# Kernel optimization log

Measured on AMD Instinct MI355X. Metric: run time of the kernel, lower is better.

## Reference

```python
import jax, jax.numpy as jnp
import numpy as np

EPS = 1e-5  # torch BatchNorm1d default eps


def setup_inputs() -> dict:
    key = jax.random.key(0)
    ks = jax.random.split(key, 8)
    F, P = 32, 64            # frames, peds per frame
    B = F * P                # batch = 2048
    E, H, M, D = 64, 128, 512, 1024  # embed, h_dim, pool_mlp_dim, bottleneck
    starts = np.arange(F, dtype=np.int64) * P
    seq_start_end = jnp.asarray(np.stack([starts, starts + P], axis=1))
    inp = {
        "curr_h_states": jax.random.normal(ks[0], (1, B, H), dtype=jnp.float32),
        "curr_pos": jax.random.normal(ks[1], (B, 2), dtype=jnp.float32),
        "seq_start_end": seq_start_end,
        # embedding: Linear(2, E)
        "We": jax.random.normal(ks[2], (2, E), dtype=jnp.float32) * 0.5,
        "be": jnp.zeros((E,), dtype=jnp.float32),
        # mlp layer 1: Linear(E+H, M) + BN(M)
        "W1": jax.random.normal(ks[3], (E + H, M), dtype=jnp.float32) * 0.05,
        "b1": jnp.zeros((M,), dtype=jnp.float32),
        "g1": jnp.ones((M,), dtype=jnp.float32),
        "beta1": jnp.zeros((M,), dtype=jnp.float32),
        # mlp layer 2: Linear(M, D) + BN(D)
        "W2": jax.random.normal(ks[4], (M, D), dtype=jnp.float32) * 0.04,
        "b2": jnp.zeros((D,), dtype=jnp.float32),
        "g2": jnp.ones((D,), dtype=jnp.float32),
        "beta2": jnp.zeros((D,), dtype=jnp.float32),
        # BN running stats (eval mode)
        "rm1": jnp.zeros((M,), dtype=jnp.float32),
        "rv1": jnp.ones((M,), dtype=jnp.float32),
        "rm2": jnp.zeros((D,), dtype=jnp.float32),
        "rv2": jnp.ones((D,), dtype=jnp.float32),
    }
    return inp


def _bn(x, g, beta, rm, rv):
    return g * (x - rm) * jax.lax.rsqrt(rv + EPS) + beta


def reference(curr_h_states, curr_pos, seq_start_end, We, be, W1, b1, g1, beta1,
              W2, b2, g2, beta2, rm1, rv1, rm2, rv2):
    # Equal-size frames: vectorize the per-frame Python loop via a reshape.
    F = seq_start_end.shape[0]
    B = curr_h_states.shape[1]
    P = B // F
    h = curr_h_states[0].reshape(F, P, -1)      # (F, P, H)
    pos = curr_pos.reshape(F, P, 2)             # (F, P, 2)
    # rel_pos[f, i, j] = pos[f, j] - pos[f, i]  (repeat minus repeat_interleave)
    rel = pos[:, None, :, :] - pos[:, :, None, :]          # (F, P, P, 2)
    emb = rel @ We + be                                     # (F, P, P, E)
    h_rep = jnp.broadcast_to(h[:, None, :, :], (F, P, P, h.shape[-1]))
    x = jnp.concatenate([emb, h_rep], axis=-1)              # (F, P, P, E+H)
    x = jax.nn.relu(_bn(x @ W1 + b1, g1, beta1, rm1, rv1))  # (F, P, P, M)
    x = jax.nn.relu(_bn(x @ W2 + b2, g2, beta2, rm2, rv2))  # (F, P, P, D)
    pool_h = x.max(axis=2)                                  # max over j -> (F, P, D)
    return pool_h.reshape(B, -1)                            # (B, D)
```

## Files before the change

kernel.cpp:

```cpp
#include <hip/hip_runtime.h>
#include <hip/hip_bf16.h>
#include <stdint.h>

#define EPS_BN 1e-5f

constexpr int Fn = 32;
constexpr int Pn = 64;
constexpr int Bn = 2048;
constexpr int Hn = 128;
constexpr int En = 64;
constexpr int Mn = 512;
constexpr int Dn = 1024;

using bf16x8  = __attribute__((ext_vector_type(8))) short;
using f32x16  = __attribute__((ext_vector_type(16))) float;

static __device__ __forceinline__ float    bcf(uint32_t u) { return __builtin_bit_cast(float, u); }
static __device__ __forceinline__ uint32_t bcu(float f)    { return __builtin_bit_cast(uint32_t, f); }
static __device__ __forceinline__ unsigned short bfbits(float f) {
  return __builtin_bit_cast(unsigned short, __float2bfloat16(f));
}

static __device__ __forceinline__ void dma16(const uint4* g, const uint4* l) {
  __builtin_amdgcn_global_load_lds(
      (const __attribute__((address_space(1))) unsigned int*)g,
      (__attribute__((address_space(3))) unsigned int*)l, 16, 0, 0);
}

static __device__ __forceinline__ bf16x8 mk_af(uint4 a, uint4 q) {
  uint4 x;
#pragma unroll
  for (int v = 0; v < 4; ++v) {
    uint32_t aw = ((const uint32_t*)&a)[v], qw = ((const uint32_t*)&q)[v];
    float lo = fmaxf(bcf(aw << 16) - bcf(qw << 16), 0.f);
    float hi = fmaxf(bcf(aw) - bcf(qw), 0.f);
    ((uint32_t*)&x)[v] = __builtin_amdgcn_perm(bcu(hi), bcu(lo), 0x07060302u);
  }
  return __builtin_bit_cast(bf16x8, x);
}

__global__ void prep_all(const float* __restrict__ hs, const float* __restrict__ pos,
                         const float* __restrict__ We, const float* __restrict__ be,
                         const float* __restrict__ W1, const float* __restrict__ b1,
                         const float* __restrict__ g1, const float* __restrict__ beta1,
                         const float* __restrict__ rm1, const float* __restrict__ rv1,
                         const float* __restrict__ W2, const float* __restrict__ b2,
                         const float* __restrict__ g2, const float* __restrict__ beta2,
                         const float* __restrict__ rm2, const float* __restrict__ rv2,
                         __hip_bfloat16* __restrict__ Agb, __hip_bfloat16* __restrict__ Qgb,
                         uint4* __restrict__ W2g, float* __restrict__ c2) {
  __shared__ float smem[64 * 65];
  int bid = blockIdx.x, t = threadIdx.x;
  if (bid < 512) {
    int rb = bid * 4, m = t;
    float* hsh = smem;
    float* psh = smem + 512;
    if (t < 4 * Hn) hsh[t] = hs[rb * Hn + t];
    if (t < 8) psh[t] = pos[rb * 2 + t];
    __syncthreads();
    float w0 = 0.f, w1 = 0.f, c = 0.f;
    for (int e = 0; e < En; ++e) {
      float w = W1[e * Mn + m];
      w0 += We[e] * w; w1 += We[En + e] * w; c += be[e] * w;
    }
    c += b1[m];
    float s  = g1[m] * rsqrtf(rv1[m] + EPS_BN);
    float tt = beta1[m] - rm1[m] * s;
    float acc[4];
#pragma unroll
    for (int ri = 0; ri < 4; ++ri) acc[ri] = c;
    for (int e = 0; e < Hn; ++e) {
      float w = W1[(En + e) * Mn + m];
#pragma unroll
      for (int ri = 0; ri < 4; ++ri) acc[ri] += hsh[ri * Hn + e] * w;
    }
#pragma unroll
    for (int ri = 0; ri < 4; ++ri) {
      float q = psh[ri * 2] * w0 + psh[ri * 2 + 1] * w1;
      Agb[(rb + ri) * Mn + m] = __float2bfloat16((acc[ri] + q) * s + tt);
      Qgb[(rb + ri) * Mn + m] = __float2bfloat16(q * s);
    }
  } else {
    int b2i = bid - 512;
    int d0 = (b2i & 15) * 64, k0 = (b2i >> 4) * 64;
    int col = t & 63, row8 = t >> 6;
#pragma unroll
    for (int rr = 0; rr < 8; ++rr) {
      int row = rr * 8 + row8;
      smem[row * 65 + col] = W2[(k0 + row) * Dn + d0 + col];
    }
    __syncthreads();
    int lane = t & 63, q8 = t >> 6;
    int sel_n = q8 & 1, sel_ks = q8 >> 1;
    int dl = sel_n * 32 + (lane & 31), d = d0 + dl;
    float sf = g2[d] * rsqrtf(rv2[d] + EPS_BN);
    int kb = sel_ks * 16 + (lane >> 5) * 8;
    uint32_t wd[4];
#pragma unroll
    for (int h = 0; h < 4; ++h) {
      uint32_t u0 = bfbits(smem[(kb + 2 * h) * 65 + dl] * sf);
      uint32_t u1 = bfbits(smem[(kb + 2 * h + 1) * 65 + dl] * sf);
      wd[h] = u0 | (u1 << 16);
    }
    int n32 = (d0 >> 5) + sel_n;
    int ks  = (k0 >> 4) + sel_ks;
    W2g[(n32 * 32 + ks) * 64 + lane] = (uint4){wd[0], wd[1], wd[2], wd[3]};
    if (k0 == 0 && t < 64) {
      int dd = d0 + t;
      float ss = g2[dd] * rsqrtf(rv2[dd] + EPS_BN);
      c2[dd] = b2[dd] * ss + beta2[dd] - rm2[dd] * ss;
    }
  }
}

__launch_bounds__(256, 2)
__global__ void gemm_pool(const __hip_bfloat16* __restrict__ Agb,
                          const __hip_bfloat16* __restrict__ Qgb,
                          const uint4* __restrict__ W2g,
                          const float* __restrict__ c2, float* __restrict__ out) {
  __shared__ uint4 SH[4096];

  int ct = blockIdx.x;
  int rt = blockIdx.y;
  int f = rt >> 4, i0 = (rt & 15) * 4;

  int t = threadIdx.x, lane = t & 63, w = t >> 6;
  int i = i0 + w;

  const uint4* Au4 = (const uint4*)(Agb + (size_t)f * Pn * Mn);
  const uint4* aGL = Au4 + (size_t)(lane & 31) * 64 + (lane >> 5);
  const uint4* bGL = W2g + (size_t)(4 * ct) * 32 * 64 + lane;
  const uint4* qP = (const uint4*)(Qgb + (size_t)(f * Pn + i) * Mn) + (lane >> 5);

#pragma unroll
  for (int s = 0; s < 8; ++s) {
    int sa = w * 8 + s;
    int kcA = sa >> 2, kst = (sa >> 1) & 1, jf = sa & 1;
    dma16(aGL + (size_t)jf * 32 * 64 + kcA * 4 + kst * 2, SH + sa * 64);
  }
#pragma unroll
  for (int s = 0; s < 8; ++s) {
    int sb = w * 8 + s;
    int kq = sb >> 2, nf = sb & 3;
    dma16(bGL + (nf * 32 + kq) * 64, SH + 2048 + sb * 64);
  }
  uint4 qc0 = qP[0], qc1 = qP[2];

  f32x16 acc[2][4];
#pragma unroll
  for (int jf = 0; jf < 2; ++jf)
#pragma unroll
    for (int nf = 0; nf < 4; ++nf)
      acc[jf][nf] = (f32x16){0.f,0.f,0.f,0.f,0.f,0.f,0.f,0.f,0.f,0.f,0.f,0.f,0.f,0.f,0.f,0.f};

  __syncthreads();

#pragma unroll
  for (int sp = 0; sp < 4; ++sp) {
    if (sp) {
      __syncthreads();
      if (sp == 2) {
#pragma unroll
        for (int s = 0; s < 8; ++s) {
          int sa = w * 8 + s;
          int kcA = sa >> 2, kst = (sa >> 1) & 1, jf = sa & 1;
          dma16(aGL + (size_t)jf * 32 * 64 + (kcA + 8) * 4 + kst * 2, SH + sa * 64);
        }
      }
#pragma unroll
      for (int s = 0; s < 8; ++s) {
        int sb = w * 8 + s;
        int kq = sb >> 2, nf = sb & 3;
        dma16(bGL + (nf * 32 + sp * 8 + kq) * 64, SH + 2048 + sb * 64);
      }
      __syncthreads();
    }
#pragma unroll
    for (int kcl = 0; kcl < 4; ++kcl) {
      int kc = sp * 4 + kcl;
      int kn = (kc < 15) ? kc + 1 : 15;
      uint4 qn0 = qP[kn * 4], qn1 = qP[kn * 4 + 2];
#pragma unroll
      for (int kst = 0; kst < 2; ++kst) {
        int aBase = (((kc & 7) * 2 + kst) * 2) * 64 + lane;
        uint4 a0 = SH[aBase];
        uint4 a1 = SH[aBase + 64];
        int bBase = 2048 + ((kcl * 2 + kst) * 4) * 64 + lane;
        uint4 q = kst ? qc1 : qc0;
        bf16x8 af0 = mk_af(a0, q);
        bf16x8 af1 = mk_af(a1, q);
#pragma unroll
        for (int nf = 0; nf < 4; ++nf) {
          bf16x8 bg = *(const bf16x8*)(SH + bBase + nf * 64);
          acc[0][nf] = __builtin_amdgcn_mfma_f32_32x32x16_bf16(af0, bg, acc[0][nf], 0, 0, 0);
          acc[1][nf] = __builtin_amdgcn_mfma_f32_32x32x16_bf16(af1, bg, acc[1][nf], 0, 0, 0);
        }
      }
      qc0 = qn0; qc1 = qn1;
    }
  }

#pragma unroll
  for (int nf = 0; nf < 4; ++nf) {
    float mx = 0.f;
#pragma unroll
    for (int jf = 0; jf < 2; ++jf)
#pragma unroll
      for (int rg = 0; rg < 16; ++rg)
        mx = fmaxf(mx, acc[jf][nf][rg]);
    mx = fmaxf(mx, __shfl_xor(mx, 32));
    if (lane < 32) {
      int d = ct * 128 + nf * 32 + (lane & 31);
      out[(f * Pn + i) * Dn + d] = fmaxf(mx + c2[d], 0.f);
    }
  }
}

extern "C" void kernel_launch(void* const* d_in, const int* in_sizes, int n_in,
                              void* d_out, int out_size, void* d_ws, size_t ws_size,
                              hipStream_t stream) {
  const float* hs    = (const float*)d_in[0];
  const float* pos   = (const float*)d_in[1];
  const float* We    = (const float*)d_in[3];
  const float* be    = (const float*)d_in[4];
  const float* W1    = (const float*)d_in[5];
  const float* b1    = (const float*)d_in[6];
  const float* g1    = (const float*)d_in[7];
  const float* beta1 = (const float*)d_in[8];
  const float* W2    = (const float*)d_in[9];
  const float* b2    = (const float*)d_in[10];
  const float* g2    = (const float*)d_in[11];
  const float* beta2 = (const float*)d_in[12];
  const float* rm1   = (const float*)d_in[13];
  const float* rv1   = (const float*)d_in[14];
  const float* rm2   = (const float*)d_in[15];
  const float* rv2   = (const float*)d_in[16];

  char* ws = (char*)d_ws;
  float* c2 = (float*)(ws + 0);
  __hip_bfloat16* Agb = (__hip_bfloat16*)(ws + 4096);
  __hip_bfloat16* Qgb = (__hip_bfloat16*)(ws + 4096 + 2097152);
  uint4* W2g = (uint4*)(ws + 4096 + 2 * 2097152);
  float* out = (float*)d_out;

  prep_all<<<640, 512, 0, stream>>>(hs, pos, We, be, W1, b1, g1, beta1, rm1, rv1,
                                    W2, b2, g2, beta2, rm2, rv2, Agb, Qgb, W2g, c2);
  gemm_pool<<<dim3(Dn / 128, (Fn * Pn * Pn) / 256), 256, 0, stream>>>(Agb, Qgb, W2g, c2, out);
}
```

Before: 250.5 us.

## Use max(A,Q) algebra with epilogue correction, double-buffer LDS staging

```diff
diff --git a/kernel.cpp b/kernel.cpp
--- a/kernel.cpp
+++ b/kernel.cpp
@@ -27,16 +27,23 @@
       (__attribute__((address_space(3))) unsigned int*)l, 16, 0, 0);
 }
 
-static __device__ __forceinline__ bf16x8 mk_af(uint4 a, uint4 q) {
-  uint4 x;
+static __device__ __forceinline__ void mk2(uint4 a0, uint4 a1, uint4 q,
+                                           bf16x8& r0, bf16x8& r1) {
+  uint4 x0, x1;
 #pragma unroll
   for (int v = 0; v < 4; ++v) {
-    uint32_t aw = ((const uint32_t*)&a)[v], qw = ((const uint32_t*)&q)[v];
-    float lo = fmaxf(bcf(aw << 16) - bcf(qw << 16), 0.f);
-    float hi = fmaxf(bcf(aw) - bcf(qw), 0.f);
-    ((uint32_t*)&x)[v] = __builtin_amdgcn_perm(bcu(hi), bcu(lo), 0x07060302u);
-  }
-  return __builtin_bit_cast(bf16x8, x);
+    uint32_t qw  = ((const uint32_t*)&q)[v];
+    uint32_t a0w = ((const uint32_t*)&a0)[v], a1w = ((const uint32_t*)&a1)[v];
+    float qlo = bcf(qw << 16);
+    float m0lo = fmaxf(bcf(a0w << 16), qlo);
+    float m1lo = fmaxf(bcf(a1w << 16), qlo);
+    float m0hi = fmaxf(bcf(a0w), bcf(qw));
+    float m1hi = fmaxf(bcf(a1w), bcf(qw));
+    ((uint32_t*)&x0)[v] = __builtin_amdgcn_perm(bcu(m0hi), bcu(m0lo), 0x07060302u);
+    ((uint32_t*)&x1)[v] = __builtin_amdgcn_perm(bcu(m1hi), bcu(m1lo), 0x07060302u);
+  }
+  r0 = __builtin_bit_cast(bf16x8, x0);
+  r1 = __builtin_bit_cast(bf16x8, x1);
 }
 
 __global__ void prep_all(const float* __restrict__ hs, const float* __restrict__ pos,
@@ -48,15 +55,17 @@
                          const float* __restrict__ g2, const float* __restrict__ beta2,
                          const float* __restrict__ rm2, const float* __restrict__ rv2,
                          __hip_bfloat16* __restrict__ Agb, __hip_bfloat16* __restrict__ Qgb,
-                         uint4* __restrict__ W2g, float* __restrict__ c2) {
+                         uint4* __restrict__ W2g, float* __restrict__ G0,
+                         float* __restrict__ G1, float* __restrict__ c2) {
   __shared__ float smem[64 * 65];
   int bid = blockIdx.x, t = threadIdx.x;
-  if (bid < 512) {
-    int rb = bid * 4, m = t;
+  if (bid < 128) {
+    int rb = bid * 16, m = t;
     float* hsh = smem;
-    float* psh = smem + 512;
-    if (t < 4 * Hn) hsh[t] = hs[rb * Hn + t];
-    if (t < 8) psh[t] = pos[rb * 2 + t];
+    float* psh = smem + 2048;
+#pragma unroll
+    for (int r4 = 0; r4 < 4; ++r4) hsh[r4 * 512 + t] = hs[rb * Hn + r4 * 512 + t];
+    if (t < 32) psh[t] = pos[rb * 2 + t];
     __syncthreads();
     float w0 = 0.f, w1 = 0.f, c = 0.f;
     for (int e = 0; e < En; ++e) {
@@ -66,22 +75,22 @@
     c += b1[m];
     float s  = g1[m] * rsqrtf(rv1[m] + EPS_BN);
     float tt = beta1[m] - rm1[m] * s;
-    float acc[4];
-#pragma unroll
-    for (int ri = 0; ri < 4; ++ri) acc[ri] = c;
+    float acc[16];
+#pragma unroll
+    for (int ri = 0; ri < 16; ++ri) acc[ri] = c;
     for (int e = 0; e < Hn; ++e) {
       float w = W1[(En + e) * Mn + m];
 #pragma unroll
-      for (int ri = 0; ri < 4; ++ri) acc[ri] += hsh[ri * Hn + e] * w;
-    }
-#pragma unroll
-    for (int ri = 0; ri < 4; ++ri) {
+      for (int ri = 0; ri < 16; ++ri) acc[ri] += hsh[ri * Hn + e] * w;
+    }
+#pragma unroll
+    for (int ri = 0; ri < 16; ++ri) {
       float q = psh[ri * 2] * w0 + psh[ri * 2 + 1] * w1;
       Agb[(rb + ri) * Mn + m] = __float2bfloat16((acc[ri] + q) * s + tt);
       Qgb[(rb + ri) * Mn + m] = __float2bfloat16(q * s);
     }
-  } else {
-    int b2i = bid - 512;
+  } else if (bid < 256) {
+    int b2i = bid - 128;
     int d0 = (b2i & 15) * 64, k0 = (b2i >> 4) * 64;
     int col = t & 63, row8 = t >> 6;
 #pragma unroll
@@ -104,11 +113,37 @@
     }
     int n32 = (d0 >> 5) + sel_n;
     int ks  = (k0 >> 4) + sel_ks;
-    W2g[(n32 * 32 + ks) * 64 + lane] = (uint4){wd[0], wd[1], wd[2], wd[3]};
-    if (k0 == 0 && t < 64) {
-      int dd = d0 + t;
-      float ss = g2[dd] * rsqrtf(rv2[dd] + EPS_BN);
-      c2[dd] = b2[dd] * ss + beta2[dd] - rm2[dd] * ss;
+    W2g[(n32 * 32 + ks) * 64 + (t & 63)] = (uint4){wd[0], wd[1], wd[2], wd[3]};
+  } else {
+    float* wr0 = smem;
+    float* wr1 = smem + 512;
+    {
+      int m = t;
+      float w0 = 0.f, w1 = 0.f;
+      for (int e = 0; e < En; ++e) {
+        float w = W1[e * Mn + m];
+        w0 += We[e] * w; w1 += We[En + e] * w;
+      }
+      float s = g1[m] * rsqrtf(rv1[m] + EPS_BN);
+      wr0[m] = w0 * s; wr1[m] = w1 * s;
+    }
+    __syncthreads();
+    float a0 = 0.f, a1 = 0.f, d0 = 0.f, d1 = 0.f;
+#pragma unroll 4
+    for (int m = 0; m < Mn; ++m) {
+      float wA = W2[m * Dn + t];
+      float wB = W2[m * Dn + t + 512];
+      a0 += wr0[m] * wA; a1 += wr1[m] * wA;
+      d0 += wr0[m] * wB; d1 += wr1[m] * wB;
+    }
+#pragma unroll
+    for (int h = 0; h < 2; ++h) {
+      int dd = t + h * 512;
+      float g0v = h ? d0 : a0, g1v = h ? d1 : a1;
+      float s2v = g2[dd] * rsqrtf(rv2[dd] + EPS_BN);
+      G0[dd] = g0v * s2v;
+      G1[dd] = g1v * s2v;
+      c2[dd] = b2[dd] * s2v + beta2[dd] - rm2[dd] * s2v;
     }
   }
 }
@@ -117,8 +152,10 @@
 __global__ void gemm_pool(const __hip_bfloat16* __restrict__ Agb,
                           const __hip_bfloat16* __restrict__ Qgb,
                           const uint4* __restrict__ W2g,
+                          const float* __restrict__ pos,
+                          const float* __restrict__ G0, const float* __restrict__ G1,
                           const float* __restrict__ c2, float* __restrict__ out) {
-  __shared__ uint4 SH[4096];
+  __shared__ uint4 SH[3072];
 
   int ct = blockIdx.x;
   int rt = blockIdx.y;
@@ -127,82 +164,88 @@
   int t = threadIdx.x, lane = t & 63, w = t >> 6;
   int i = i0 + w;
 
-  const uint4* Au4 = (const uint4*)(Agb + (size_t)f * Pn * Mn);
-  const uint4* aGL = Au4 + (size_t)(lane & 31) * 64 + (lane >> 5);
+  const uint4* aGL = (const uint4*)(Agb + (size_t)f * Pn * Mn) +
+                     (size_t)(lane & 31) * 64 + (lane >> 5);
   const uint4* bGL = W2g + (size_t)(4 * ct) * 32 * 64 + lane;
-  const uint4* qP = (const uint4*)(Qgb + (size_t)(f * Pn + i) * Mn) + (lane >> 5);
-
-#pragma unroll
-  for (int s = 0; s < 8; ++s) {
-    int sa = w * 8 + s;
-    int kcA = sa >> 2, kst = (sa >> 1) & 1, jf = sa & 1;
-    dma16(aGL + (size_t)jf * 32 * 64 + kcA * 4 + kst * 2, SH + sa * 64);
-  }
-#pragma unroll
-  for (int s = 0; s < 8; ++s) {
-    int sb = w * 8 + s;
-    int kq = sb >> 2, nf = sb & 3;
-    dma16(bGL + (nf * 32 + kq) * 64, SH + 2048 + sb * 64);
-  }
+  const uint4* qP  = (const uint4*)(Qgb + (size_t)(f * Pn + i) * Mn) + (lane >> 5);
+  float px = pos[(f * Pn + i) * 2], py = pos[(f * Pn + i) * 2 + 1];
+
+  auto stage = [&](int p) {
+    int buf = p & 1;
+#pragma unroll
+    for (int s6 = 0; s6 < 6; ++s6) {
+      int s = w * 6 + s6;
+      if (s < 8) {
+        int kcl = s >> 2, kst = (s >> 1) & 1, jf = s & 1;
+        dma16(aGL + (size_t)jf * 2048 + (p * 2 + kcl) * 4 + kst * 2,
+              SH + buf * 512 + s * 64);
+      } else {
+        int sb = s - 8, kq = sb >> 2, nf = sb & 3;
+        dma16(bGL + (nf * 32 + p * 4 + kq) * 64,
+              SH + 1024 + buf * 1024 + sb * 64);
+      }
+    }
+  };
+
+  f32x16 acc[2][4];
+#pragma unroll
+  for (int jf = 0; jf < 2; ++jf)
+#pragma unroll
+    for (int nf = 0; nf < 4; ++nf)
+      acc[jf][nf] = (f32x16){0.f,0.f,0.f,0.f,0.f,0.f,0.f,0.f,
+                             0.f,0.f,0.f,0.f,0.f,0.f,0.f,0.f};
+
+  stage(0);
   uint4 qc0 = qP[0], qc1 = qP[2];
-
-  f32x16 acc[2][4];
-#pragma unroll
-  for (int jf = 0; jf < 2; ++jf)
-#pragma unroll
-    for (int nf = 0; nf < 4; ++nf)
-      acc[jf][nf] = (f32x16){0.f,0.f,0.f,0.f,0.f,0.f,0.f,0.f,0.f,0.f,0.f,0.f,0.f,0.f,0.f,0.f};
-
-  __syncthreads();
-
-#pragma unroll
-  for (int sp = 0; sp < 4; ++sp) {
-    if (sp) {
-      __syncthreads();
-      if (sp == 2) {
-#pragma unroll
-        for (int s = 0; s < 8; ++s) {
-          int sa = w * 8 + s;
-          int kcA = sa >> 2, kst = (sa >> 1) & 1, jf = sa & 1;
-          dma16(aGL + (size_t)jf * 32 * 64 + (kcA + 8) * 4 + kst * 2, SH + sa * 64);
-        }
-      }
-#pragma unroll
-      for (int s = 0; s < 8; ++s) {
-        int sb = w * 8 + s;
-        int kq = sb >> 2, nf = sb & 3;
-        dma16(bGL + (nf * 32 + sp * 8 + kq) * 64, SH + 2048 + sb * 64);
-      }
-      __syncthreads();
-    }
-#pragma unroll
-    for (int kcl = 0; kcl < 4; ++kcl) {
-      int kc = sp * 4 + kcl;
-      int kn = (kc < 15) ? kc + 1 : 15;
-      uint4 qn0 = qP[kn * 4], qn1 = qP[kn * 4 + 2];
-#pragma unroll
-      for (int kst = 0; kst < 2; ++kst) {
-        int aBase = (((kc & 7) * 2 + kst) * 2) * 64 + lane;
-        uint4 a0 = SH[aBase];
-        uint4 a1 = SH[aBase + 64];
-        int bBase = 2048 + ((kcl * 2 + kst) * 4) * 64 + lane;
-        uint4 q = kst ? qc1 : qc0;
-        bf16x8 af0 = mk_af(a0, q);
-        bf16x8 af1 = mk_af(a1, q);
-#pragma unroll
-        for (int nf = 0; nf < 4; ++nf) {
-          bf16x8 bg = *(const bf16x8*)(SH + bBase + nf * 64);
-          acc[0][nf] = __builtin_amdgcn_mfma_f32_32x32x16_bf16(af0, bg, acc[0][nf], 0, 0, 0);
-          acc[1][nf] = __builtin_amdgcn_mfma_f32_32x32x16_bf16(af1, bg, acc[1][nf], 0, 0, 0);
-        }
-      }
-      qc0 = qn0; qc1 = qn1;
+  uint4 qn0, qn1;
+
+#pragma unroll
+  for (int p = 0; p < 8; ++p) {
+    __syncthreads();
+    if (p < 7) stage(p + 1);
+    int abase = (p & 1) * 512 + lane;
+    int bbase = 1024 + (p & 1) * 1024 + lane;
+
+    uint4 cA0 = SH[abase], cA1 = SH[abase + 64];
+    uint4 cB[4];
+#pragma unroll
+    for (int nf = 0; nf < 4; ++nf) cB[nf] = SH[bbase + nf * 64];
+
+#pragma unroll
+    for (int ks = 0; ks < 4; ++ks) {
+      uint4 nA0, nA1, nB[4];
+      if (ks < 3) {
+        nA0 = SH[abase + (ks + 1) * 128];
+        nA1 = SH[abase + (ks + 1) * 128 + 64];
+#pragma unroll
+        for (int nf = 0; nf < 4; ++nf) nB[nf] = SH[bbase + ((ks + 1) * 4 + nf) * 64];
+      }
+      if (ks == 0) { qn0 = qP[(p * 2 + 1) * 4]; qn1 = qP[(p * 2 + 1) * 4 + 2]; }
+      if (ks == 2) {
+        int knc = (p < 7) ? p * 2 + 2 : 15;
+        qn0 = qP[knc * 4]; qn1 = qP[knc * 4 + 2];
+      }
+
+      bf16x8 af0, af1;
+      mk2(cA0, cA1, (ks & 1) ? qc1 : qc0, af0, af1);
+#pragma unroll
+      for (int nf = 0; nf < 4; ++nf) {
+        bf16x8 bg = __builtin_bit_cast(bf16x8, cB[nf]);
+        acc[0][nf] = __builtin_amdgcn_mfma_f32_32x32x16_bf16(af0, bg, acc[0][nf], 0, 0, 0);
+        acc[1][nf] = __builtin_amdgcn_mfma_f32_32x32x16_bf16(af1, bg, acc[1][nf], 0, 0, 0);
+      }
+      if (ks & 1) { qc0 = qn0; qc1 = qn1; }
+      if (ks < 3) {
+        cA0 = nA0; cA1 = nA1;
+#pragma unroll
+        for (int nf = 0; nf < 4; ++nf) cB[nf] = nB[nf];
+      }
     }
   }
 
 #pragma unroll
   for (int nf = 0; nf < 4; ++nf) {
-    float mx = 0.f;
+    float mx = -3.0e38f;
 #pragma unroll
     for (int jf = 0; jf < 2; ++jf)
 #pragma unroll
@@ -211,7 +254,8 @@
     mx = fmaxf(mx, __shfl_xor(mx, 32));
     if (lane < 32) {
       int d = ct * 128 + nf * 32 + (lane & 31);
-      out[(f * Pn + i) * Dn + d] = fmaxf(mx + c2[d], 0.f);
+      float r = px * G0[d] + py * G1[d];
+      out[(f * Pn + i) * Dn + d] = fmaxf(mx - r + c2[d], 0.f);
     }
   }
 }
@@ -238,12 +282,16 @@
 
   char* ws = (char*)d_ws;
   float* c2 = (float*)(ws + 0);
-  __hip_bfloat16* Agb = (__hip_bfloat16*)(ws + 4096);
-  __hip_bfloat16* Qgb = (__hip_bfloat16*)(ws + 4096 + 2097152);
-  uint4* W2g = (uint4*)(ws + 4096 + 2 * 2097152);
+  float* G0 = (float*)(ws + 4096);
+  float* G1 = (float*)(ws + 8192);
+  __hip_bfloat16* Agb = (__hip_bfloat16*)(ws + 12288);
+  __hip_bfloat16* Qgb = (__hip_bfloat16*)(ws + 12288 + 2097152);
+  uint4* W2g = (uint4*)(ws + 12288 + 2 * 2097152);
   float* out = (float*)d_out;
 
-  prep_all<<<640, 512, 0, stream>>>(hs, pos, We, be, W1, b1, g1, beta1, rm1, rv1,
-                                    W2, b2, g2, beta2, rm2, rv2, Agb, Qgb, W2g, c2);
-  gemm_pool<<<dim3(Dn / 128, (Fn * Pn * Pn) / 256), 256, 0, stream>>>(Agb, Qgb, W2g, c2, out);
-}
+  prep_all<<<257, 512, 0, stream>>>(hs, pos, We, be, W1, b1, g1, beta1, rm1, rv1,
+                                    W2, b2, g2, beta2, rm2, rv2, Agb, Qgb, W2g,
+                                    G0, G1, c2);
+  gemm_pool<<<dim3(Dn / 128, (Fn * Pn * Pn) / 256), 256, 0, stream>>>(
+      Agb, Qgb, W2g, pos, G0, G1, c2, out);
+}
```

After: 300.0 us. 19.8% more time.
